# Kernel tuning notes

Hardware: AMD Instinct MI355X
Metric: run time of the kernel (lower is better)

## Reference

```python
import jax, jax.numpy as jnp
import numpy as np

DIM = 384
DIM_HEAD = 32
HEADS = DIM // DIM_HEAD  # 12
WIN = 8
DIM_FF = 1536
FUSED = DIM + DIM + DIM_FF  # 2304


def setup_inputs() -> dict:
    key = jax.random.key(0)
    ks = jax.random.split(key, 8)
    B, H, W = 16, 64, 64
    x = jax.random.normal(ks[0], (B, DIM, H, W), dtype=jnp.float32)
    s = lambda fan_in: 1.0 / np.sqrt(fan_in)
    w_fused = jax.random.normal(ks[1], (FUSED, DIM), dtype=jnp.float32) * s(DIM)
    w_gate = jax.random.normal(ks[2], (HEADS, DIM), dtype=jnp.float32) * s(DIM)
    b_gate = jnp.full((HEADS,), 0.5, dtype=jnp.float32)  # init_constant_(0.5)
    w_attn_out = jax.random.normal(ks[3], (DIM, DIM), dtype=jnp.float32) * s(DIM)
    w_ff_out = jax.random.normal(ks[4], (DIM, DIM_FF), dtype=jnp.float32) * s(DIM_FF)
    # StarReLU learnable scalars (metaformer defaults)
    sr_scale = jnp.asarray(0.8944, dtype=jnp.float32)
    sr_bias = jnp.asarray(-0.4472, dtype=jnp.float32)
    return {"x": x, "w_fused": w_fused, "w_gate": w_gate, "b_gate": b_gate,
            "w_attn_out": w_attn_out, "w_ff_out": w_ff_out,
            "sr_scale": sr_scale, "sr_bias": sr_bias}


def reference(x, w_fused, w_gate, b_gate, w_attn_out, w_ff_out, sr_scale, sr_bias):
    B, C, H, W = x.shape
    p = WIN
    gh, gw = H // p, W // p
    n = p * p
    # b c (h p1) (w p2) -> (b h w) (p1 p2) c
    xw = x.reshape(B, C, gh, p, gw, p).transpose(0, 2, 4, 3, 5, 1).reshape(B * gh * gw, n, C)
    fused = jnp.einsum('bnc,fc->bnf', xw, w_fused)  # [Bw, n, 2304]
    q, kv, x_ff = jnp.split(fused, [DIM, 2 * DIM], axis=-1)
    # b n (h d) -> b h n d
    q = q.reshape(-1, n, HEADS, DIM_HEAD).transpose(0, 2, 1, 3)
    kv = kv.reshape(-1, n, HEADS, DIM_HEAD).transpose(0, 2, 1, 3)
    scale = 1.0 / np.sqrt(DIM_HEAD)
    scores = jnp.einsum('bhnd,bhmd->bhnm', q, kv) * scale
    attn = jax.nn.softmax(scores, axis=-1)
    x_attn = jnp.einsum('bhnm,bhmd->bhnd', attn, kv)  # kv is both key and value
    gate = jnp.einsum('bnc,hc->bnh', xw, w_gate) + b_gate  # [Bw, n, heads]
    x_attn = x_attn * jax.nn.sigmoid(gate.transpose(0, 2, 1)[..., None])
    x_attn = x_attn.transpose(0, 2, 1, 3).reshape(-1, n, DIM)
    ff = sr_scale * jnp.square(jax.nn.relu(x_ff)) + sr_bias  # StarReLU
    out = jnp.einsum('bnc,oc->bno', x_attn, w_attn_out) + jnp.einsum('bnf,of->bno', ff, w_ff_out)
    # (b h w) (p1 p2) c -> b c (h p1) (w p2)
    out = out.reshape(B, gh, gw, p, p, C).transpose(0, 5, 1, 3, 2, 4).reshape(B, C, H, W)
    return out
```

## Files before the change

kernel.cpp:

```cpp
#include <hip/hip_runtime.h>
#include <hip/hip_bf16.h>

typedef __bf16 bf16x8 __attribute__((ext_vector_type(8), may_alias));
typedef float f32x4 __attribute__((ext_vector_type(4), may_alias));
typedef unsigned short ushort_a __attribute__((may_alias));
typedef unsigned int uint_a __attribute__((may_alias));
typedef unsigned short us8 __attribute__((ext_vector_type(8), may_alias));

#define MFMA(a, b, c) __builtin_amdgcn_mfma_f32_16x16x32_bf16(a, b, c, 0, 0, 0)

__device__ __forceinline__ unsigned short f2bf(float f) {
  return __builtin_bit_cast(unsigned short, (__bf16)f);
}
__device__ __forceinline__ float bf2f(unsigned short u) {
  unsigned v = ((unsigned)u) << 16;
  return __builtin_bit_cast(float, v);
}

__device__ __forceinline__ void kbar() {
  __builtin_amdgcn_sched_barrier(0);
  asm volatile("s_waitcnt lgkmcnt(0)" ::: "memory");
  __builtin_amdgcn_sched_barrier(0);
  __builtin_amdgcn_s_barrier();
  __builtin_amdgcn_sched_barrier(0);
}

#define GLOAD(G, L)                                                          \
  __builtin_amdgcn_global_load_lds(                                          \
      (const __attribute__((address_space(1))) unsigned int*)(G),            \
      (__attribute__((address_space(3))) unsigned int*)(L), 16, 0, 0)

#define OFF_WG 884736
#define OFF_WAO 933888
#define OFF_WFO 1081344
#define OFF_XG 1671168
#define OFF_FUSED 26836992
#define OFF_GATE 177831936

__global__ __launch_bounds__(256) void prep_weights(
    const float* __restrict__ wf, const float* __restrict__ wg,
    const float* __restrict__ wao, const float* __restrict__ wfo,
    unsigned short* __restrict__ ws) {
  int i = blockIdx.x * 256 + threadIdx.x;
  if (i < 884736) { ws[i] = f2bf(wf[i]); return; }
  int j = i - 884736;
  if (j < 49152) { ws[i] = f2bf(j < 4608 ? wg[j] : 0.0f); return; }
  j -= 49152;
  if (j < 147456) { ws[i] = f2bf(wao[j]); return; }
  j -= 147456;
  if (j < 589824) ws[i] = f2bf(wfo[j]);
}

__global__ __launch_bounds__(256) void k0_gather(const float* __restrict__ x,
                                                 unsigned short* __restrict__ xg) {
  __shared__ __align__(16) char As[49152];
  int tid = threadIdx.x, wi = blockIdx.x;
  int b = wi >> 6, ghi = (wi >> 3) & 7, gwi = wi & 7;
  const float* xb = x + (size_t)b * 1572864 + (ghi * 8) * 64 + gwi * 8;
  for (int it = 0; it < 12; ++it) {
    int idx = it * 256 + tid;
    int c = idx % 384, p1 = idx / 384;
    const float* src = xb + (size_t)c * 4096 + p1 * 64;
    float4 v0 = *(const float4*)src, v1 = *(const float4*)(src + 4);
    float f[8] = {v0.x, v0.y, v0.z, v0.w, v1.x, v1.y, v1.z, v1.w};
#pragma unroll
    for (int jj = 0; jj < 8; ++jj) {
      int row = p1 * 8 + jj;
      int byte = (row * 768 + c * 2) ^ ((row & 7) << 4);
      *(ushort_a*)(As + byte) = f2bf(f[jj]);
    }
  }
  __syncthreads();
  unsigned short* og = xg + (size_t)wi * 24576;
#pragma unroll
  for (int it = 0; it < 12; ++it) {
    int idx = it * 256 + tid;
    int row = idx / 48, c = idx % 48;
    int byte = (row * 768 + c * 16) ^ ((row & 7) << 4);
    *(us8*)(og + (size_t)row * 384 + c * 8) = *(us8*)(As + byte);
  }
}

__global__ __launch_bounds__(512, 4) void k1_gemm(unsigned short* __restrict__ ws,
                                                  const float* __restrict__ srs,
                                                  const float* __restrict__ srb) {
  __shared__ __align__(16) char sm[65536];
  const int tid = threadIdx.x, lane = tid & 63, wave = tid >> 6;
  const int l15 = lane & 15, l4 = lane >> 4;
  const int wr = wave & 3, wc = wave >> 2;
  const int bid = blockIdx.x;
  const int swz = (bid & 7) * 1216 + (bid >> 3);
  const int mb = swz / 19, nb = swz - mb * 19;
  const unsigned short* Ab = ws + OFF_XG + (size_t)mb * 128 * 384;
  const unsigned short* Bb =
      (nb < 18) ? ws + (size_t)nb * 128 * 384 : ws + OFF_WG;
  const int srow = tid >> 3, sc = tid & 7;
  f32x4 of[2][4] = {};
  us8 sA0[2], sB0[2], sA1[2], sB1[2];

#define K1_LOAD(KS, SA, SB)                                                   \
  {                                                                           \
    _Pragma("unroll") for (int r2 = 0; r2 < 2; ++r2) {                        \
      int row = srow + 64 * r2;                                               \
      SA[r2] = *(const us8*)(Ab + (size_t)row * 384 + (KS)*64 + sc * 8);      \
      SB[r2] = *(const us8*)(Bb + (size_t)row * 384 + (KS)*64 + sc * 8);      \
    }                                                                         \
  }
#define K1_WRITE(BUF, SA, SB)                                                 \
  {                                                                           \
    _Pragma("unroll") for (int r2 = 0; r2 < 2; ++r2) {                        \
      int row = srow + 64 * r2;                                               \
      int byte = ((row * 128 + sc * 16) ^ ((row & 7) << 4)) + (BUF);          \
      *(us8*)(sm + byte) = SA[r2];                                            \
      *(us8*)(sm + 32768 + byte) = SB[r2];                                    \
    }                                                                         \
  }
#define K1_COMPUTE(BUF)                                                       \
  {                                                                           \
    _Pragma("unroll") for (int kk = 0; kk < 2; ++kk) {                        \
      bf16x8 af[2], bfr[4];                                                   \
      _Pragma("unroll") for (int mt = 0; mt < 2; ++mt) {                      \
        int row = wr * 32 + mt * 16 + l15;                                    \
        af[mt] = *(const bf16x8*)(sm + (BUF) +                                \
                 ((row * 128 + kk * 64 + l4 * 16) ^ ((row & 7) << 4)));       \
      }                                                                       \
      _Pragma("unroll") for (int nt = 0; nt < 4; ++nt) {                      \
        int row = wc * 64 + nt * 16 + l15;                                    \
        bfr[nt] = *(const bf16x8*)(sm + 32768 + (BUF) +                       \
                  ((row * 128 + kk * 64 + l4 * 16) ^ ((row & 7) << 4)));      \
      }                                                                       \
      _Pragma("unroll") for (int mt = 0; mt < 2; ++mt)                        \
      _Pragma("unroll") for (int nt = 0; nt < 4; ++nt)                        \
          of[mt][nt] = MFMA(af[mt], bfr[nt], of[mt][nt]);                     \
    }                                                                         \
  }

  K1_LOAD(0, sA0, sB0);
  K1_LOAD(1, sA1, sB1);
  K1_WRITE(0, sA0, sB0);
  __syncthreads();
#pragma unroll 1
  for (int kp = 0; kp < 3; ++kp) {
    int ks = kp * 2;
    if (ks + 2 < 6) K1_LOAD(ks + 2, sA0, sB0);
    K1_COMPUTE(0);
    K1_WRITE(16384, sA1, sB1);
    kbar();
    if (ks + 3 < 6) K1_LOAD(ks + 3, sA1, sB1);
    K1_COMPUTE(16384);
    if (ks + 2 < 6) K1_WRITE(0, sA0, sB0);
    kbar();
  }
  const float ssc = srs[0], sbi = srb[0];
  const bool ffreg = (nb >= 6) && (nb < 18);
#pragma unroll
  for (int mt = 0; mt < 2; ++mt)
#pragma unroll
    for (int nt = 0; nt < 4; ++nt)
#pragma unroll
      for (int rr = 0; rr < 4; ++rr) {
        int row = wr * 32 + mt * 16 + l4 * 4 + rr;
        int col = wc * 64 + nt * 16 + l15;
        float v = of[mt][nt][rr];
        if (ffreg) { v = fmaxf(v, 0.0f); v = ssc * v * v + sbi; }
        *(ushort_a*)(sm + ((row * 256 + col * 2) ^ ((row & 7) << 4))) = f2bf(v);
      }
  __syncthreads();
  if (nb < 18) {
    unsigned short* fo = ws + OFF_FUSED + (size_t)mb * 128 * 2304 + nb * 128;
#pragma unroll
    for (int r2 = 0; r2 < 4; ++r2) {
      int idx = r2 * 512 + tid;
      int row = idx >> 4, c = idx & 15;
      int byte = (row * 256 + c * 16) ^ ((row & 7) << 4);
      *(us8*)(fo + (size_t)row * 2304 + c * 8) = *(us8*)(sm + byte);
    }
  } else {
    unsigned short* go = ws + OFF_GATE + (size_t)mb * 128 * 16;
#pragma unroll
    for (int r2 = 0; r2 < 4; ++r2) {
      int idx = r2 * 512 + tid;
      int row = idx >> 4, c = idx & 15;
      if (c < 2) {
        int byte = (row * 256 + c * 16) ^ ((row & 7) << 4);
        *(us8*)(go + (size_t)row * 16 + c * 8) = *(us8*)(sm + byte);
      }
    }
  }
}

__global__ __launch_bounds__(256, 3) void k2_attn(unsigned short* __restrict__ ws,
                                                  const float* __restrict__ bgate) {
  __shared__ __align__(16) char sm[49152];
  const int tid = threadIdx.x, lane = tid & 63, wave = tid >> 6;
  const int l15 = lane & 15, l4 = lane >> 4;
  char* kvT = sm + wave * 12288;
  char* Pb = kvT + 4096;
  const int wi = blockIdx.x;
  const size_t T0 = (size_t)wi * 64;
  unsigned short* fused = ws + OFF_FUSED;
  const unsigned short* gb = ws + OFF_GATE;
  const f32x4 zz = {};
#pragma unroll 1
  for (int hi = 0; hi < 3; ++hi) {
    const int h = wave + hi * 4;
    bf16x8 akv[4], bq[4];
#pragma unroll
    for (int t = 0; t < 4; ++t) {
      akv[t] = *(const bf16x8*)(fused + (T0 + t * 16 + l15) * 2304 + 384 + h * 32 + l4 * 8);
      bq[t] = *(const bf16x8*)(fused + (T0 + t * 16 + l15) * 2304 + h * 32 + l4 * 8);
    }
    f32x4 sfT[4][4];
#pragma unroll
    for (int mt = 0; mt < 4; ++mt)
#pragma unroll
      for (int ni = 0; ni < 4; ++ni) sfT[mt][ni] = MFMA(akv[mt], bq[ni], zz);
#pragma unroll
    for (int mt = 0; mt < 4; ++mt) {
      us8 u = __builtin_bit_cast(us8, akv[mt]);
      int m = mt * 16 + l15;
#pragma unroll
      for (int j = 0; j < 8; ++j) {
        int d = l4 * 8 + j;
        *(ushort_a*)(kvT + ((d * 128 + m * 2) ^ ((d & 7) << 4))) = u[j];
      }
    }
#pragma unroll
    for (int ni = 0; ni < 4; ++ni) {
      float s[16];
#pragma unroll
      for (int mt = 0; mt < 4; ++mt)
#pragma unroll
        for (int rr = 0; rr < 4; ++rr)
          s[mt * 4 + rr] = sfT[mt][ni][rr] * 0.176776695f;
      float mx = s[0];
#pragma unroll
      for (int q2 = 1; q2 < 16; ++q2) mx = fmaxf(mx, s[q2]);
      mx = fmaxf(mx, __shfl_xor(mx, 16, 64));
      mx = fmaxf(mx, __shfl_xor(mx, 32, 64));
      float sum = 0.0f;
#pragma unroll
      for (int q2 = 0; q2 < 16; ++q2) {
        s[q2] = __expf(s[q2] - mx);
        sum += s[q2];
      }
      sum += __shfl_xor(sum, 16, 64);
      sum += __shfl_xor(sum, 32, 64);
      float rs = 1.0f / sum;
      int n = ni * 16 + l15;
      int rowb = n * 128, sw = (n & 7) << 4;
#pragma unroll
      for (int mt = 0; mt < 4; ++mt) {
        int m = mt * 16 + l4 * 4;
        unsigned p0 = (unsigned)f2bf(s[mt * 4 + 0] * rs) |
                      ((unsigned)f2bf(s[mt * 4 + 1] * rs) << 16);
        unsigned p1 = (unsigned)f2bf(s[mt * 4 + 2] * rs) |
                      ((unsigned)f2bf(s[mt * 4 + 3] * rs) << 16);
        *(uint_a*)(Pb + ((rowb + m * 2) ^ sw)) = p0;
        *(uint_a*)(Pb + ((rowb + (m + 2) * 2) ^ sw)) = p1;
      }
    }
    f32x4 xo[4][2] = {};
#pragma unroll
    for (int ks = 0; ks < 2; ++ks) {
      bf16x8 bv[2];
#pragma unroll
      for (int dt = 0; dt < 2; ++dt) {
        int d = dt * 16 + l15;
        bv[dt] = *(const bf16x8*)(kvT + ((d * 128 + ks * 64 + l4 * 16) ^ ((d & 7) << 4)));
      }
#pragma unroll
      for (int nt = 0; nt < 4; ++nt) {
        int n = nt * 16 + l15;
        bf16x8 ap = *(const bf16x8*)(Pb + ((n * 128 + ks * 64 + l4 * 16) ^ ((n & 7) << 4)));
        xo[nt][0] = MFMA(ap, bv[0], xo[nt][0]);
        xo[nt][1] = MFMA(ap, bv[1], xo[nt][1]);
      }
    }
    const float bgh = bgate[h];
#pragma unroll
    for (int nt = 0; nt < 4; ++nt)
#pragma unroll
      for (int rr = 0; rr < 4; ++rr) {
        int n = nt * 16 + l4 * 4 + rr;
        float gv = bf2f(gb[(T0 + n) * 16 + h]) + bgh;
        float sg = 1.0f / (1.0f + __expf(-gv));
#pragma unroll
        for (int dt = 0; dt < 2; ++dt)
          fused[(T0 + n) * 2304 + h * 32 + dt * 16 + l15] =
              f2bf(xo[nt][dt][rr] * sg);
      }
  }
}

__global__ __launch_bounds__(256, 2) void k3_gemm(const unsigned short* __restrict__ ws,
                                                  float* __restrict__ out) {
  __shared__ __align__(1024) char sm[65536];
  const int tid = threadIdx.x, lane = tid & 63, wave = tid >> 6;
  const int l15 = lane & 15, l4 = lane >> 4;
  const int wr = wave & 1, wc = wave >> 1;
  const int bid = blockIdx.x;
  const int swz = (bid & 7) * 192 + (bid >> 3);
  const int mb = 511 - swz / 3, nB = swz % 3;
  const size_t T0 = (size_t)mb * 128;
  const unsigned short* fA = ws + OFF_FUSED + T0 * 2304;
  const unsigned short* wao = ws + OFF_WAO + (size_t)(nB * 128) * 384;
  const unsigned short* wfo = ws + OFF_WFO + (size_t)(nB * 128) * 1536;
  const int lr = lane >> 3, lc = (lane & 7) ^ lr;
  const int offA = lr * 2304 + lc * 8;
  const int offB384 = lr * 384 + lc * 8;
  const int offB1536 = lr * 1536 + lc * 8;
  f32x4 of[4][4] = {};

#define K3_STAGE(KS, BUF)                                                     \
  {                                                                           \
    const int ac_ = (KS) < 6 ? (KS)*64 : 768 + ((KS)-6) * 64;                 \
    _Pragma("unroll") for (int i = 0; i < 4; ++i) {                           \
      const int R = wave * 32 + i * 8;                                        \
      GLOAD(fA + (size_t)R * 2304 + ac_ + offA, sm + (BUF) + R * 128);        \
      if ((KS) < 6)                                                           \
        GLOAD(wao + (size_t)R * 384 + (KS)*64 + offB384,                      \
              sm + 32768 + (BUF) + R * 128);                                  \
      else                                                                    \
        GLOAD(wfo + (size_t)R * 1536 + ((KS)-6) * 64 + offB1536,              \
              sm + 32768 + (BUF) + R * 128);                                  \
    }                                                                         \
  }

  K3_STAGE(0, 0);
#pragma unroll 1
  for (int ks = 0; ks < 30; ++ks) {
    const int cur = (ks & 1) * 16384;
    if (ks + 1 < 30) K3_STAGE(ks + 1, 16384 - cur);
    __builtin_amdgcn_sched_barrier(0);
    if (ks + 1 < 30)
      asm volatile("s_waitcnt vmcnt(8)" ::: "memory");
    else
      asm volatile("s_waitcnt vmcnt(0)" ::: "memory");
    __builtin_amdgcn_sched_barrier(0);
    __builtin_amdgcn_s_barrier();
    __builtin_amdgcn_sched_barrier(0);
#pragma unroll
    for (int kk = 0; kk < 2; ++kk) {
      bf16x8 af[4], bfr[4];
#pragma unroll
      for (int mt = 0; mt < 4; ++mt) {
        int row = wr * 64 + mt * 16 + l15;
        af[mt] = *(const bf16x8*)(sm + cur +
                 ((row * 128 + kk * 64 + l4 * 16) ^ ((row & 7) << 4)));
      }
#pragma unroll
      for (int nt = 0; nt < 4; ++nt) {
        int row = wc * 64 + nt * 16 + l15;
        bfr[nt] = *(const bf16x8*)(sm + 32768 + cur +
                  ((row * 128 + kk * 64 + l4 * 16) ^ ((row & 7) << 4)));
      }
#pragma unroll
      for (int mt = 0; mt < 4; ++mt)
#pragma unroll
        for (int nt = 0; nt < 4; ++nt)
          of[mt][nt] = MFMA(af[mt], bfr[nt], of[mt][nt]);
    }
    kbar();
  }
#pragma unroll
  for (int mt = 0; mt < 4; ++mt) {
    int n0 = wr * 64 + mt * 16 + l4 * 4;
    int T = (int)T0 + n0;
    int wi = T >> 6, n = T & 63;
    int b = wi >> 6, ghi = (wi >> 3) & 7, gwi = wi & 7;
    float* ob = out + (size_t)b * 1572864 + (size_t)(ghi * 8 + (n >> 3)) * 64 +
                gwi * 8 + (n & 7);
#pragma unroll
    for (int nt = 0; nt < 4; ++nt) {
      int c = nB * 128 + wc * 64 + nt * 16 + l15;
      __builtin_nontemporal_store(of[mt][nt], (f32x4*)(ob + (size_t)c * 4096));
    }
  }
}

extern "C" void kernel_launch(void* const* d_in, const int* in_sizes, int n_in,
                              void* d_out, int out_size, void* d_ws, size_t ws_size,
                              hipStream_t stream) {
  const float* x = (const float*)d_in[0];
  const float* wf = (const float*)d_in[1];
  const float* wg = (const float*)d_in[2];
  const float* bg = (const float*)d_in[3];
  const float* wao = (const float*)d_in[4];
  const float* wfo = (const float*)d_in[5];
  const float* srs = (const float*)d_in[6];
  const float* srb = (const float*)d_in[7];
  unsigned short* ws = (unsigned short*)d_ws;

  prep_weights<<<6528, 256, 0, stream>>>(wf, wg, wao, wfo, ws);
  k0_gather<<<1024, 256, 0, stream>>>(x, ws + OFF_XG);
  k1_gemm<<<512 * 19, 512, 0, stream>>>(ws, srs, srb);
  k2_attn<<<1024, 256, 0, stream>>>(ws, bg);
  k3_gemm<<<512 * 3, 256, 0, stream>>>(ws, (float*)d_out);
}
```

Baseline: 482.5 us.

## Use direct global-to-LDS loads with double buffering in fused projection GEMM

Replaces the register-staged global loads and LDS writes in the first GEMM with direct global-to-LDS loads (GLOAD), using lane-level XOR pre-swizzled source offsets so the LDS layout stays compatible with the swizzled reads. The k-loop becomes a simple double-buffered pipeline with vmcnt waits and a barrier per step. It also changes launch bounds from 4 to 2 blocks per SM hint, freeing registers. This removes the VGPR round-trip and ds_write instructions, but relies on the GLOAD macro's async path and vmcnt accounting being correct.

```diff
diff --git a/kernel.cpp b/kernel.cpp
--- a/kernel.cpp
+++ b/kernel.cpp
@@ -81,10 +81,10 @@
   }
 }
 
-__global__ __launch_bounds__(512, 4) void k1_gemm(unsigned short* __restrict__ ws,
+__global__ __launch_bounds__(512, 2) void k1_gemm(unsigned short* __restrict__ ws,
                                                   const float* __restrict__ srs,
                                                   const float* __restrict__ srb) {
-  __shared__ __align__(16) char sm[65536];
+  __shared__ __align__(1024) char sm[65536];
   const int tid = threadIdx.x, lane = tid & 63, wave = tid >> 6;
   const int l15 = lane & 15, l4 = lane >> 4;
   const int wr = wave & 3, wc = wave >> 2;
@@ -94,61 +94,54 @@
   const unsigned short* Ab = ws + OFF_XG + (size_t)mb * 128 * 384;
   const unsigned short* Bb =
       (nb < 18) ? ws + (size_t)nb * 128 * 384 : ws + OFF_WG;
-  const int srow = tid >> 3, sc = tid & 7;
+  const int lr = lane >> 3, lc = (lane & 7) ^ lr;
+  const int offS = lr * 384 + lc * 8;
   f32x4 of[2][4] = {};
-  us8 sA0[2], sB0[2], sA1[2], sB1[2];
-
-#define K1_LOAD(KS, SA, SB)                                                   \
+
+#define K1_STAGE(KS, BUF)                                                     \
   {                                                                           \
-    _Pragma("unroll") for (int r2 = 0; r2 < 2; ++r2) {                        \
-      int row = srow + 64 * r2;                                               \
-      SA[r2] = *(const us8*)(Ab + (size_t)row * 384 + (KS)*64 + sc * 8);      \
-      SB[r2] = *(const us8*)(Bb + (size_t)row * 384 + (KS)*64 + sc * 8);      \
+    _Pragma("unroll") for (int i = 0; i < 2; ++i) {                           \
+      const int R = wave * 16 + i * 8;                                        \
+      GLOAD(Ab + (size_t)R * 384 + (KS)*64 + offS, sm + (BUF) + R * 128);     \
+      GLOAD(Bb + (size_t)R * 384 + (KS)*64 + offS,                            \
+            sm + 32768 + (BUF) + R * 128);                                    \
     }                                                                         \
   }
-#define K1_WRITE(BUF, SA, SB)                                                 \
-  {                                                                           \
-    _Pragma("unroll") for (int r2 = 0; r2 < 2; ++r2) {                        \
-      int row = srow + 64 * r2;                                               \
-      int byte = ((row * 128 + sc * 16) ^ ((row & 7) << 4)) + (BUF);          \
-      *(us8*)(sm + byte) = SA[r2];                                            \
-      *(us8*)(sm + 32768 + byte) = SB[r2];                                    \
-    }                                                                         \
-  }
-#define K1_COMPUTE(BUF)                                                       \
-  {                                                                           \
-    _Pragma("unroll") for (int kk = 0; kk < 2; ++kk) {                        \
-      bf16x8 af[2], bfr[4];                                                   \
-      _Pragma("unroll") for (int mt = 0; mt < 2; ++mt) {                      \
-        int row = wr * 32 + mt * 16 + l15;                                    \
-        af[mt] = *(const bf16x8*)(sm + (BUF) +                                \
-                 ((row * 128 + kk * 64 + l4 * 16) ^ ((row & 7) << 4)));       \
-      }                                                                       \
-      _Pragma("unroll") for (int nt = 0; nt < 4; ++nt) {                      \
-        int row = wc * 64 + nt * 16 + l15;                                    \
-        bfr[nt] = *(const bf16x8*)(sm + 32768 + (BUF) +                       \
-                  ((row * 128 + kk * 64 + l4 * 16) ^ ((row & 7) << 4)));      \
-      }                                                                       \
-      _Pragma("unroll") for (int mt = 0; mt < 2; ++mt)                        \
-      _Pragma("unroll") for (int nt = 0; nt < 4; ++nt)                        \
-          of[mt][nt] = MFMA(af[mt], bfr[nt], of[mt][nt]);                     \
-    }                                                                         \
-  }
-
-  K1_LOAD(0, sA0, sB0);
-  K1_LOAD(1, sA1, sB1);
-  K1_WRITE(0, sA0, sB0);
-  __syncthreads();
+
+  K1_STAGE(0, 0);
 #pragma unroll 1
-  for (int kp = 0; kp < 3; ++kp) {
-    int ks = kp * 2;
-    if (ks + 2 < 6) K1_LOAD(ks + 2, sA0, sB0);
-    K1_COMPUTE(0);
-    K1_WRITE(16384, sA1, sB1);
-    kbar();
-    if (ks + 3 < 6) K1_LOAD(ks + 3, sA1, sB1);
-    K1_COMPUTE(16384);
-    if (ks + 2 < 6) K1_WRITE(0, sA0, sB0);
+  for (int ks = 0; ks < 6; ++ks) {
+    const int cur = (ks & 1) * 16384;
+    if (ks + 1 < 6) K1_STAGE(ks + 1, 16384 - cur);
+    __builtin_amdgcn_sched_barrier(0);
+    if (ks + 1 < 6)
+      asm volatile("s_waitcnt vmcnt(4)" ::: "memory");
+    else
+      asm volatile("s_waitcnt vmcnt(0)" ::: "memory");
+    __builtin_amdgcn_sched_barrier(0);
+    __builtin_amdgcn_s_barrier();
+    __builtin_amdgcn_sched_barrier(0);
+#pragma unroll
+    for (int kk = 0; kk < 2; ++kk) {
+      bf16x8 af[2], bfr[4];
+#pragma unroll
+      for (int mt = 0; mt < 2; ++mt) {
+        int row = wr * 32 + mt * 16 + l15;
+        af[mt] = *(const bf16x8*)(sm + cur +
+                 ((row * 128 + kk * 64 + l4 * 16) ^ ((row & 7) << 4)));
+      }
+#pragma unroll
+      for (int nt = 0; nt < 4; ++nt) {
+        int row = wc * 64 + nt * 16 + l15;
+        bfr[nt] = *(const bf16x8*)(sm + 32768 + cur +
+                  ((row * 128 + kk * 64 + l4 * 16) ^ ((row & 7) << 4)));
+      }
+#pragma unroll
+      for (int mt = 0; mt < 2; ++mt)
+#pragma unroll
+        for (int nt = 0; nt < 4; ++nt)
+          of[mt][nt] = MFMA(af[mt], bfr[nt], of[mt][nt]);
+    }
     kbar();
   }
   const float ssc = srs[0], sbi = srb[0];
```

Measured after the change: 489.7 us. No clear change (+1.5%).
